# Kernel optimization log

Hardware: AMD Instinct MI355X
Metric: run time of the kernel (lower is better)

## Reference

```python
import jax, jax.numpy as jnp
import numpy as np
from jax import lax

EPS_BN = 1e-5
EPS_LN = 1e-5
IMG = 240
BETA = 1.0

def l2norm(x, axis=-1):
    n = jnp.linalg.norm(x, axis=axis, keepdims=True)
    return x / jnp.maximum(n, 1e-12)

def bn2d(x, g, b):
    # training-mode BatchNorm2d: stats over (B,H,W), biased variance
    m = x.mean(axis=(0, 2, 3), keepdims=True)
    v = x.var(axis=(0, 2, 3), keepdims=True)
    return g[None, :, None, None] * (x - m) * lax.rsqrt(v + EPS_BN) + b[None, :, None, None]

def conv2d(x, w):
    return lax.conv_general_dilated(x, w, (1, 1), 'SAME', dimension_numbers=('NCHW', 'OIHW', 'NCHW'))

def convT2x2(x, w, b):
    # ConvTranspose2d k=2 s=2 pad=0; torch weight layout (C_in, C_out, 2, 2)
    B, C, H, W = x.shape
    O = w.shape[1]
    y = jnp.einsum('bchw,copq->bohpwq', x, w).reshape(B, O, 2 * H, 2 * W)
    return y + b[None, :, None, None]

def layernorm(x, g, b):
    m = x.mean(-1, keepdims=True)
    v = x.var(-1, keepdims=True)
    return g * (x - m) * lax.rsqrt(v + EPS_LN) + b

def setup_inputs() -> dict:
    key = jax.random.key(0)
    ks = jax.random.split(key, 12)
    L, B, K, N, D = 3, 16, 8, 256, 768
    H, MID = 128, 64
    inp = {
        'query': jax.random.normal(ks[0], (L, B, N, D), jnp.float32),
        'prompt': jax.random.normal(ks[1], (L, B, K, N, D), jnp.float32),
        'sharebn_g': jnp.ones((L, D)), 'sharebn_b': jnp.zeros((L, D)),
        'lw1': 0.02 * jax.random.normal(ks[2], (L, H, D, 3, 3)),
        'lbn1g': jnp.ones((L, H)), 'lbn1b': jnp.zeros((L, H)),
        'lwt1': 0.05 * jax.random.normal(ks[3], (L, H, H, 2, 2)), 'lbt1': jnp.zeros((L, H)),
        'lw2': 0.02 * jax.random.normal(ks[4], (L, MID, H, 3, 3)),
        'lbn2g': jnp.ones((L, MID)), 'lbn2b': jnp.zeros((L, MID)),
        'lwt2': 0.05 * jax.random.normal(ks[5], (L, MID, MID, 2, 2)), 'lbt2': jnp.zeros((L, MID)),
        'lw3': 0.05 * jax.random.normal(ks[6], (L, 2, MID, 1, 1)), 'lb3': jnp.zeros((L, 2)),
        'pool_logits': jnp.zeros((L, 2)),
        'mw1': 0.02 * jax.random.normal(ks[7], (L, H, D)),
        'mlng': jnp.ones((L, H)), 'mlnb': jnp.zeros((L, H)),
        'mw2': 0.05 * jax.random.normal(ks[8], (L, 2, H)), 'mb2': jnp.zeros((L, 2)),
    }
    return inp

def _layer(q, pf, p):
    # q: [B,N,D], pf: [B,M,D]
    B, N, D = q.shape
    g = int(N ** 0.5)
    qn = l2norm(q)
    pn = l2norm(pf)
    sim = jnp.einsum('bnc,bmc->bnm', qn, pn)              # [B,N,M]
    max_cos = sim.max(axis=-1)
    idx = sim.argmax(axis=-1)                              # [B,N]
    aligned = jnp.take_along_axis(pf, idx[:, :, None], axis=1)  # [B,N,D]
    residual = 0.5 * (1.0 - max_cos)
    an = l2norm(aligned)
    ctx = qn + BETA * jnp.abs(qn - an)                     # [B,N,D]
    cmap = ctx.transpose(0, 2, 1).reshape(B, D, g, g)
    cmap = bn2d(cmap, p['sbg'], p['sbb'])
    # local conv head
    x = jax.nn.relu(bn2d(conv2d(cmap, p['w1']), p['bn1g'], p['bn1b']))
    x = convT2x2(x, p['wt1'], p['bt1'])
    x = jax.nn.relu(bn2d(conv2d(x, p['w2']), p['bn2g'], p['bn2b']))
    x = convT2x2(x, p['wt2'], p['bt2'])
    raw = conv2d(x, p['w3']) + p['b3'][None, :, None, None]   # [B,2,4g,4g]
    # adaptive_avg_pool2d 4g -> g (exact 4x4 blocks)
    pl2c = raw.reshape(B, 2, g, 4, g, 4).mean(axis=(3, 5))    # [B,2,g,g]
    ps2c = jax.nn.softmax(pl2c, axis=1)
    patch_logits = (pl2c[:, 1] - pl2c[:, 0]).reshape(B, -1)
    patch_scores = ps2c[:, 1].reshape(B, -1)
    local_logits = jax.image.resize(raw, (B, 2, IMG, IMG), method='bilinear')
    # global head (GAP/GMP fusion over context map features)
    cf = cmap.reshape(B, D, N)
    gap = cf.mean(axis=-1)
    gmp = cf.max(axis=-1)
    pw = jax.nn.softmax(p['pl'])
    pooled = pw[0] * gap + pw[1] * gmp                     # [B,D]
    h = jax.nn.relu(layernorm(pooled @ p['mw1'].T, p['lng'], p['lnb']))
    logits2 = h @ p['mw2'].T + p['mb2']
    glogit = logits2[:, 1] - logits2[:, 0]
    return residual, patch_scores, patch_logits, glogit, local_logits, pw, idx, aligned

def reference(query, prompt, sharebn_g, sharebn_b, lw1, lbn1g, lbn1b, lwt1, lbt1,
              lw2, lbn2g, lbn2b, lwt2, lbt2, lw3, lb3, pool_logits,
              mw1, mlng, mlnb, mw2, mb2):
    L, B = query.shape[0], query.shape[1]
    outs = []
    for l in range(L):
        pf = prompt[l].reshape(B, -1, prompt.shape[-1])
        p = dict(sbg=sharebn_g[l], sbb=sharebn_b[l], w1=lw1[l], bn1g=lbn1g[l], bn1b=lbn1b[l],
                 wt1=lwt1[l], bt1=lbt1[l], w2=lw2[l], bn2g=lbn2g[l], bn2b=lbn2b[l],
                 wt2=lwt2[l], bt2=lbt2[l], w3=lw3[l], b3=lb3[l], pl=pool_logits[l],
                 mw1=mw1[l], lng=mlng[l], lnb=mlnb[l], mw2=mw2[l], mb2=mb2[l])
        outs.append(_layer(query[l], pf, p))
    stacked = tuple(jnp.stack([o[i] for o in outs]) for i in range(8))
    return stacked
```

## Files before the change

### kernel.cpp

```cpp
#include <hip/hip_runtime.h>
#include <hip/hip_bf16.h>
#include <math.h>

#define LLY 3
#define BB 16
#define NNQ 256
#define DD 768
#define MMP 2048
#define HH 128
#define MD 64
#define IMGSZ 240
#define LBTOT (LLY*BB)

#define OFF_INVQ 0
#define OFF_INVP (OFF_INVQ + LLY*BB*NNQ)
#define OFF_CMAP (OFF_INVP + LLY*BB*MMP)
#define OFF_BNSH (OFF_CMAP + LLY*BB*DD*NNQ)
#define OFF_X1   (OFF_BNSH + 2*LLY*DD)
#define OFF_BN1  (OFF_X1 + LLY*BB*HH*256)
#define OFF_T1   (OFF_BN1 + 2*LLY*HH)
#define OFF_X2   (OFF_T1 + LLY*BB*HH*1024)
#define OFF_BN2  (OFF_X2 + LLY*BB*MD*1024)
#define OFF_T2   (OFF_BN2 + 2*LLY*MD)
#define OFF_RAW3 (OFF_T2 + LLY*BB*MD*4096)
#define WS_FLOATS (OFF_RAW3 + LLY*BB*2*4096)
#define T1BSH (LBTOT*1024*HH)
#define SQH   (LBTOT*NNQ*DD)
#define OFF_C1P (OFF_T2 + 4718592)
#define OFF_C2P (OFF_T2 + 3256320)
#define OFF_PGL 0
#define X1B_SH 0
#define WT1B_SH 1600000

#define O_RES 0
#define O_PSC (O_RES + LLY*BB*NNQ)
#define O_PLG (O_PSC + LLY*BB*NNQ)
#define O_GLG (O_PLG + LLY*BB*NNQ)
#define O_LOC (O_GLG + LLY*BB)
#define O_PW  (O_LOC + LLY*BB*2*IMGSZ*IMGSZ)
#define O_IDX (O_PW + LLY*2)
#define O_ALN (O_IDX + LLY*BB*NNQ)

typedef __attribute__((ext_vector_type(8))) short bf16x8;
typedef __attribute__((ext_vector_type(4))) float f32x4;

__device__ __forceinline__ unsigned short f2bf(float f) {
    __hip_bfloat16 h = __float2bfloat16(f);
    unsigned short u;
    __builtin_memcpy(&u, &h, sizeof(u));
    return u;
}
__device__ __forceinline__ float bf2f(unsigned short h) {
    return __uint_as_float(((unsigned int)h) << 16);
}

__device__ __forceinline__ float blockReduceSum(float v, float* sm) {
    for (int o = 32; o; o >>= 1) v += __shfl_down(v, o, 64);
    __syncthreads();
    if ((threadIdx.x & 63) == 0) sm[threadIdx.x >> 6] = v;
    __syncthreads();
    return sm[0] + sm[1] + sm[2] + sm[3];
}

__global__ __launch_bounds__(192) void knormq(const float* __restrict__ query,
                                              float* __restrict__ ws) {
    __shared__ float sm[3];
    int row = blockIdx.x;
    int t = threadIdx.x;
    float4 v = *(const float4*)(query + (size_t)row * DD + t * 4);
    float ss = v.x * v.x + v.y * v.y + v.z * v.z + v.w * v.w;
    for (int o = 32; o; o >>= 1) ss += __shfl_down(ss, o, 64);
    if ((t & 63) == 0) sm[t >> 6] = ss;
    __syncthreads();
    ss = sm[0] + sm[1] + sm[2];
    float iv = 1.0f / fmaxf(sqrtf(ss), 1e-12f);
    if (t == 0) ws[OFF_INVQ + row] = iv;
    unsigned short* qh = (unsigned short*)(ws + OFF_T2);
    unsigned short* ql = qh + SQH;
    float e[4] = {v.x * iv, v.y * iv, v.z * iv, v.w * iv};
    unsigned int hp[2], lp[2];
    #pragma unroll
    for (int j = 0; j < 2; j++) {
        unsigned short h0 = f2bf(e[2*j]), h1 = f2bf(e[2*j+1]);
        unsigned short l0 = f2bf(e[2*j] - bf2f(h0)), l1 = f2bf(e[2*j+1] - bf2f(h1));
        hp[j] = (unsigned int)h0 | ((unsigned int)h1 << 16);
        lp[j] = (unsigned int)l0 | ((unsigned int)l1 << 16);
    }
    *(uint2*)(qh + (size_t)row * DD + t * 4) = make_uint2(hp[0], hp[1]);
    *(uint2*)(ql + (size_t)row * DD + t * 4) = make_uint2(lp[0], lp[1]);
}

__global__ __launch_bounds__(512) void ksimm(const float* __restrict__ prompt, float* __restrict__ ws) {
    __shared__ __align__(16) unsigned short Ah[128][40];
    __shared__ __align__(16) unsigned short Al[128][40];
    __shared__ __align__(16) unsigned short Bh[256][40];
    __shared__ __align__(16) unsigned short Bl[256][40];
    __shared__ float invL[128];
    int bid = blockIdx.x;
    int mt = bid & 15;
    int lb = bid >> 4;
    int t = threadIdx.x;
    int lane = t & 63, wave = t >> 6;
    int wm = wave >> 2, wn = wave & 3;
    int fr = lane & 15, fq = lane >> 4;
    const unsigned short* qh = (const unsigned short*)(ws + OFF_T2);
    const unsigned short* ql = qh + SQH;
    const float* pbase = prompt + (size_t)lb * MMP * DD + (size_t)(mt * 128) * DD;

    float ssq[2] = {0.f, 0.f};

    f32x4 acc[4][4];
    #pragma unroll
    for (int mi = 0; mi < 4; mi++)
        #pragma unroll
        for (int ni = 0; ni < 4; ni++) acc[mi][ni] = (f32x4){0.f, 0.f, 0.f, 0.f};

    for (int kc = 0; kc < DD; kc += 32) {
        __syncthreads();
        #pragma unroll
        for (int i = 0; i < 2; i++) {
            int f = t + i * 512;
            int row = f >> 3, c4 = f & 7;
            float4 v = *(const float4*)(pbase + (size_t)row * DD + kc + c4 * 4);
            ssq[i] += v.x * v.x + v.y * v.y + v.z * v.z + v.w * v.w;
            unsigned short h0 = f2bf(v.x), h1 = f2bf(v.y), h2 = f2bf(v.z), h3 = f2bf(v.w);
            unsigned short l0 = f2bf(v.x - bf2f(h0)), l1 = f2bf(v.y - bf2f(h1));
            unsigned short l2 = f2bf(v.z - bf2f(h2)), l3 = f2bf(v.w - bf2f(h3));
            uint2 hp = make_uint2((unsigned int)h0 | ((unsigned int)h1 << 16),
                                  (unsigned int)h2 | ((unsigned int)h3 << 16));
            uint2 lp = make_uint2((unsigned int)l0 | ((unsigned int)l1 << 16),
                                  (unsigned int)l2 | ((unsigned int)l3 << 16));
            *(uint2*)&Ah[row][c4 * 4] = hp;
            *(uint2*)&Al[row][c4 * 4] = lp;
        }
        #pragma unroll
        for (int i = 0; i < 2; i++) {
            int f = t + i * 512;
            int row = f >> 2, sg = f & 3;
            size_t go = (size_t)(lb * NNQ + row) * DD + kc + sg * 8;
            *(uint4*)&Bh[row][sg * 8] = *(const uint4*)(qh + go);
            *(uint4*)&Bl[row][sg * 8] = *(const uint4*)(ql + go);
        }
        __syncthreads();
        bf16x8 ah[4], al4[4], bh[4], bl4[4];
        #pragma unroll
        for (int mi = 0; mi < 4; mi++) {
            ah[mi]  = *(const bf16x8*)&Ah[wm * 64 + mi * 16 + fr][fq * 8];
            al4[mi] = *(const bf16x8*)&Al[wm * 64 + mi * 16 + fr][fq * 8];
        }
        #pragma unroll
        for (int ni = 0; ni < 4; ni++) {
            bh[ni]  = *(const bf16x8*)&Bh[wn * 64 + ni * 16 + fr][fq * 8];
            bl4[ni] = *(const bf16x8*)&Bl[wn * 64 + ni * 16 + fr][fq * 8];
        }
        #pragma unroll
        for (int mi = 0; mi < 4; mi++)
            #pragma unroll
            for (int ni = 0; ni < 4; ni++) {
                acc[mi][ni] = __builtin_amdgcn_mfma_f32_16x16x32_bf16(ah[mi],  bh[ni],  acc[mi][ni], 0, 0, 0);
                acc[mi][ni] = __builtin_amdgcn_mfma_f32_16x16x32_bf16(ah[mi],  bl4[ni], acc[mi][ni], 0, 0, 0);
                acc[mi][ni] = __builtin_amdgcn_mfma_f32_16x16x32_bf16(al4[mi], bh[ni],  acc[mi][ni], 0, 0, 0);
            }
    }
    #pragma unroll
    for (int i = 0; i < 2; i++) {
        float s = ssq[i];
        s += __shfl_xor(s, 1, 64);
        s += __shfl_xor(s, 2, 64);
        s += __shfl_xor(s, 4, 64);
        if ((t & 7) == 0) {
            int row = (t >> 3) + 64 * i;
            float iv = 1.0f / fmaxf(sqrtf(s), 1e-12f);
            invL[row] = iv;
            ws[OFF_INVP + lb * MMP + mt * 128 + row] = iv;
        }
    }
    __syncthreads();
    float* bestv = ws + OFF_X1;
    float* besti = ws + OFF_X1 + (size_t)LBTOT * NNQ * 32;
    #pragma unroll
    for (int ni = 0; ni < 4; ni++) {
        float bv = -1e30f; int bi = 0;
        #pragma unroll
        for (int mi = 0; mi < 4; mi++)
            #pragma unroll
            for (int rr = 0; rr < 4; rr++) {
                int lm = wm * 64 + mi * 16 + fq * 4 + rr;
                float s = acc[mi][ni][rr] * invL[lm];
                int m = mt * 128 + lm;
                if (s > bv) { bv = s; bi = m; }
            }
        #pragma unroll
        for (int o = 16; o <= 32; o <<= 1) {
            float ov = __shfl_xor(bv, o, 64);
            int oi = __shfl_xor(bi, o, 64);
            if (ov > bv || (ov == bv && oi < bi)) { bv = ov; bi = oi; }
        }
        if (fq == 0) {
            int q = wn * 64 + ni * 16 + fr;
            size_t slot = (size_t)(lb * NNQ + q) * 32 + wm * 16 + mt;
            bestv[slot] = bv;
            besti[slot] = (float)bi;
        }
    }
}

__global__ __launch_bounds__(256) void kpost(const float* __restrict__ query,
                                             const float* __restrict__ prompt,
                                             float* __restrict__ ws,
                                             float* __restrict__ out) {
    __shared__ float red_v[16];
    __shared__ int   red_i[16];
    __shared__ float Lctx[DD * 17];
    int bid = blockIdx.x;
    int nt = bid & 15;
    int lb = bid >> 4;
    int t = threadIdx.x;
    const float* bestv = ws + OFF_X1;
    const float* besti = ws + OFF_X1 + (size_t)LBTOT * NNQ * 32;
    if (t < 16) {
        int q = nt * 16 + t;
        const float* bv = bestv + (size_t)(lb * NNQ + q) * 32;
        const float* bi = besti + (size_t)(lb * NNQ + q) * 32;
        float best = -1e30f; int bidx2 = 0;
        for (int mtt = 0; mtt < 16; mtt++)
            #pragma unroll
            for (int wm = 0; wm < 2; wm++) {
                float v = bv[wm * 16 + mtt];
                if (v > best) { best = v; bidx2 = (int)bi[wm * 16 + mtt]; }
            }
        red_v[t] = best; red_i[t] = bidx2;
        out[O_RES + lb * NNQ + q] = 0.5f * (1.0f - best);
        out[O_IDX + lb * NNQ + q] = (float)bidx2;
    }
    __syncthreads();
    const float* qbase = query + (size_t)(lb * NNQ + nt * 16) * DD;
    const float* pbase = prompt + (size_t)lb * MMP * DD;
    const float* invq = ws + OFF_INVQ + lb * NNQ + nt * 16;
    const float* invp = ws + OFF_INVP + lb * MMP;
    int c = t & 15;
    int nn = t >> 4;
    int gn = nt * 16 + nn;
    int midx = red_i[nn];
    float ip = invp[midx];
    float iq = invq[nn];
    const float* prow = pbase + (size_t)midx * DD;
    const float* qrow = qbase + (size_t)nn * DD;
    float* aln = out + O_ALN + (size_t)(lb * NNQ + gn) * DD;
    for (int jj = 0; jj < DD / 16; jj++) {
        int d = c + jj * 16;
        float pvr = prow[d];
        float qv = qrow[d] * iq;
        float av = pvr * ip;
        float cx = qv + fabsf(qv - av);
        aln[d] = pvr;
        Lctx[d * 17 + nn] = cx;
    }
    __syncthreads();
    float* cm = ws + OFF_CMAP + (size_t)lb * DD * NNQ + nt * 16;
    int nl = t & 15, dd = t >> 4;
    for (int jj = 0; jj < DD / 16; jj++) {
        int d = jj * 16 + dd;
        cm[(size_t)d * NNQ + nl] = Lctx[d * 17 + nl];
    }
    {
        float* pp = ws + OFF_C1P + (size_t)(lb * 16 + nt) * (DD * 4);
        #pragma unroll
        for (int k = 0; k < 3; k++) {
            int d = t * 3 + k;
            float s = 0.f, sq = 0.f, mx = -1e30f, mn = 1e30f;
            #pragma unroll
            for (int n2 = 0; n2 < 16; n2++) {
                float v = Lctx[d * 17 + n2];
                s += v; sq += v * v;
                mx = fmaxf(mx, v); mn = fminf(mn, v);
            }
            pp[d] = s;
            pp[DD + d] = sq;
            pp[2 * DD + d] = mx;
            pp[3 * DD + d] = mn;
        }
    }
}

__global__ __launch_bounds__(256) void kbnfin(const float* __restrict__ g,
                                              const float* __restrict__ b,
                                              float* __restrict__ ws) {
    __shared__ float ssm[4][64], sqm[4][64];
    int chunk = blockIdx.x % 12;
    int l = blockIdx.x / 12;
    int t = threadIdx.x;
    int d = chunk * 64 + (t & 63);
    int r = t >> 6;
    float s = 0.f, sq = 0.f;
    for (int j = r; j < 256; j += 4) {
        const float* pp = ws + OFF_C1P + (size_t)(l * 256 + j) * (DD * 4);
        s += pp[d];
        sq += pp[DD + d];
    }
    ssm[r][t & 63] = s; sqm[r][t & 63] = sq;
    __syncthreads();
    if (r == 0) {
        s  = ssm[0][t] + ssm[1][t] + ssm[2][t] + ssm[3][t];
        sq = sqm[0][t] + sqm[1][t] + sqm[2][t] + sqm[3][t];
        float inv = 1.0f / 4096.f;
        float m = s * inv;
        float var = sq * inv - m * m;
        float sc = g[l * DD + d] * rsqrtf(var + 1e-5f);
        float bo = b[l * DD + d] - m * sc;
        ws[OFF_BNSH + l * DD + d] = sc;
        ws[OFF_BNSH + LLY * DD + l * DD + d] = bo;
    }
}

__global__ __launch_bounds__(64) void kgapf(float* __restrict__ ws,
                                            const float* __restrict__ pool_logits) {
    int chunk = blockIdx.x % 12;
    int lb = blockIdx.x / 12;
    int l = lb >> 4;
    int t = threadIdx.x;
    int d = chunk * 64 + t;
    float s = 0.f, mx = -1e30f, mn = 1e30f;
    for (int nt = 0; nt < 16; nt++) {
        const float* pp = ws + OFF_C1P + (size_t)(lb * 16 + nt) * (DD * 4);
        s += pp[d];
        mx = fmaxf(mx, pp[2 * DD + d]);
        mn = fminf(mn, pp[3 * DD + d]);
    }
    float p0 = pool_logits[l * 2], p1 = pool_logits[l * 2 + 1];
    float mxp = fmaxf(p0, p1);
    float e0 = expf(p0 - mxp), e1 = expf(p1 - mxp);
    float pw0 = e0 / (e0 + e1), pw1 = e1 / (e0 + e1);
    float sc = ws[OFF_BNSH + l * DD + d];
    float bo = ws[OFF_BNSH + LLY * DD + l * DD + d];
    float gap = sc * (s * (1.f / NNQ)) + bo;
    float gmp = (sc >= 0.f) ? (sc * mx + bo) : (sc * mn + bo);
    ws[OFF_PGL + lb * DD + d] = pw0 * gap + pw1 * gmp;
}

__global__ __launch_bounds__(256) void kbnstats(const float* __restrict__ x, int C, int SP,
                                                const float* __restrict__ g,
                                                const float* __restrict__ b,
                                                float* __restrict__ outSB) {
    __shared__ float sm[4];
    int bid = blockIdx.x;
    int c = bid % C;
    int l = bid / C;
    int t = threadIdx.x;
    float s = 0.f, sq = 0.f;
    for (int bb2 = 0; bb2 < BB; ++bb2) {
        const float* p = x + ((size_t)(l * BB + bb2) * C + c) * SP;
        for (int i = t; i < SP; i += 256) { float v = p[i]; s += v; sq += v * v; }
    }
    s = blockReduceSum(s, sm);
    sq = blockReduceSum(sq, sm);
    if (t == 0) {
        float inv = 1.0f / (float)(BB * SP);
        float m = s * inv;
        float var = sq * inv - m * m;
        float sc = g[l * C + c] * rsqrtf(var + 1e-5f);
        float bo = b[l * C + c] - m * sc;
        outSB[l * C + c] = sc;
        outSB[LLY * C + l * C + c] = bo;
    }
}

__global__ __launch_bounds__(256) void kw1cvt(const float* __restrict__ lw1, float* __restrict__ ws) {
    unsigned short* w1B = (unsigned short*)(ws + OFF_X2);
    int bid = blockIdx.x;
    int l = bid / HH, co = bid % HH;
    int t = threadIdx.x;
    for (int c0 = 0; c0 < DD; c0 += 256) {
        int ci = c0 + t;
        const float* src = lw1 + ((size_t)(l * HH + co) * DD + ci) * 9;
        #pragma unroll
        for (int tap = 0; tap < 9; tap++) {
            w1B[((size_t)((l * 9 + tap) * HH + co)) * DD + ci] = f2bf(src[tap]);
        }
    }
}

__global__ __launch_bounds__(256) void kbn1cvt(float* __restrict__ ws) {
    __shared__ float Ld[64][65];
    unsigned short* cmT = (unsigned short*)(ws + OFF_T2);
    int bid = blockIdx.x;
    int nt = bid & 3;
    int r = bid >> 2;
    int ct = r % 12;
    int lb = r / 12;
    int l = lb >> 4;
    int t = threadIdx.x;
    const float* cmap = ws + OFF_CMAP + (size_t)lb * DD * NNQ;
    const float* bns = ws + OFF_BNSH + l * DD;
    const float* bnb = ws + OFF_BNSH + LLY * DD + l * DD;
    #pragma unroll
    for (int i = 0; i < 4; i++) {
        int f = t + i * 256;
        int row = f >> 4, c4 = f & 15;
        int ci = ct * 64 + row;
        float4 v = *(const float4*)(cmap + (size_t)ci * NNQ + nt * 64 + c4 * 4);
        float s = bns[ci], bo = bnb[ci];
        Ld[row][c4*4+0] = v.x * s + bo; Ld[row][c4*4+1] = v.y * s + bo;
        Ld[row][c4*4+2] = v.z * s + bo; Ld[row][c4*4+3] = v.w * s + bo;
    }
    __syncthreads();
    #pragma unroll
    for (int i = 0; i < 2; i++) {
        int f = t + i * 256;
        int row = f >> 3, seg = f & 7;
        unsigned int pk[4];
        #pragma unroll
        for (int e = 0; e < 4; e++) {
            unsigned int lo = f2bf(Ld[seg * 8 + 2 * e][row]);
            unsigned int hi = f2bf(Ld[seg * 8 + 2 * e + 1][row]);
            pk[e] = lo | (hi << 16);
        }
        uint4 o = make_uint4(pk[0], pk[1], pk[2], pk[3]);
        *(uint4*)(cmT + ((size_t)(lb * NNQ + nt * 64 + row)) * DD + ct * 64 + seg * 8) = o;
    }
}

__global__ __launch_bounds__(256) void kconv1m(float* __restrict__ ws) {
    __shared__ __align__(16) unsigned short Ab[128][72];
    __shared__ __align__(16) unsigned short Bb[128][72];
    int bid = blockIdx.x;
    int s = bid % 6;
    int ntile = (bid / 6) & 1;
    int lb = bid / 12;
    int l = lb >> 4;
    int t = threadIdx.x;
    int lane = t & 63;
    int wave = t >> 6;
    int wr = wave >> 1, wc = wave & 1;
    int fr = lane & 15, fq = lane >> 4;
    const unsigned short* w1B = (const unsigned short*)(ws + OFF_X2);
    const unsigned short* cmT = (const unsigned short*)(ws + OFF_T2);

    f32x4 acc[4][4];
    #pragma unroll
    for (int mi = 0; mi < 4; mi++)
        #pragma unroll
        for (int ni = 0; ni < 4; ni++) acc[mi][ni] = (f32x4){0.f, 0.f, 0.f, 0.f};

    for (int g = s * 18; g < s * 18 + 18; ++g) {
        int tap = g / 12;
        int kc = (g % 12) * 64;
        int dy = tap / 3 - 1, dx = tap % 3 - 1;
        const unsigned short* wpl = w1B + (size_t)((l * 9 + tap) * HH) * DD;
        __syncthreads();
        #pragma unroll
        for (int i = 0; i < 4; i++) {
            int f = t + i * 256;
            int row = f >> 3, seg = f & 7;
            uint4 v = *(const uint4*)(wpl + (size_t)row * DD + kc + seg * 8);
            *(uint4*)&Ab[row][seg * 8] = v;
        }
        #pragma unroll
        for (int i = 0; i < 4; i++) {
            int f = t + i * 256;
            int row = f >> 3, seg = f & 7;
            int n = ntile * 128 + row;
            int y = (n >> 4) + dy, x = (n & 15) + dx;
            bool ok = ((unsigned)y < 16u) && ((unsigned)x < 16u);
            uint4 v = make_uint4(0u, 0u, 0u, 0u);
            if (ok) v = *(const uint4*)(cmT + ((size_t)(lb * NNQ + y * 16 + x)) * DD + kc + seg * 8);
            *(uint4*)&Bb[row][seg * 8] = v;
        }
        __syncthreads();
        #pragma unroll
        for (int kk = 0; kk < 64; kk += 32) {
            bf16x8 af[4], bfv[4];
            #pragma unroll
            for (int mi = 0; mi < 4; mi++)
                af[mi] = *(const bf16x8*)&Ab[wr * 64 + mi * 16 + fr][kk + fq * 8];
            #pragma unroll
            for (int ni = 0; ni < 4; ni++)
                bfv[ni] = *(const bf16x8*)&Bb[wc * 64 + ni * 16 + fr][kk + fq * 8];
            #pragma unroll
            for (int mi = 0; mi < 4; mi++)
                #pragma unroll
                for (int ni = 0; ni < 4; ni++)
                    acc[mi][ni] = __builtin_amdgcn_mfma_f32_16x16x32_bf16(af[mi], bfv[ni], acc[mi][ni], 0, 0, 0);
        }
    }
    float* dst = (s == 5) ? (ws + OFF_X1 + (size_t)lb * HH * 256)
                          : (ws + OFF_C1P + (size_t)(s * LBTOT + lb) * (HH * 256));
    #pragma unroll
    for (int mi = 0; mi < 4; mi++) {
        #pragma unroll
        for (int ni = 0; ni < 4; ni++) {
            int gn = ntile * 128 + wc * 64 + ni * 16 + fr;
            #pragma unroll
            for (int rr = 0; rr < 4; rr++) {
                int co = wr * 64 + mi * 16 + fq * 4 + rr;
                dst[(size_t)co * 256 + gn] = acc[mi][ni][rr];
            }
        }
    }
}

__global__ __launch_bounds__(256) void kc1red(float* __restrict__ ws) {
    size_t i = ((size_t)blockIdx.x * 256 + threadIdx.x) * 8;
    float4 a0 = *(float4*)(ws + OFF_X1 + i);
    float4 a1 = *(float4*)(ws + OFF_X1 + i + 4);
    #pragma unroll
    for (int s = 0; s < 5; s++) {
        const float* p = ws + OFF_C1P + (size_t)s * (LBTOT * HH * 256) + i;
        float4 b0 = *(const float4*)p;
        float4 b1 = *(const float4*)(p + 4);
        a0.x += b0.x; a0.y += b0.y; a0.z += b0.z; a0.w += b0.w;
        a1.x += b1.x; a1.y += b1.y; a1.z += b1.z; a1.w += b1.w;
    }
    *(float4*)(ws + OFF_X1 + i) = a0;
    *(float4*)(ws + OFF_X1 + i + 4) = a1;
}

__global__ __launch_bounds__(256) void kxcvt(const float* __restrict__ x,
                                             const float* __restrict__ sbsb,
                                             unsigned short* __restrict__ xb,
                                             int CI, int SPIN, int nT, int cT) {
    __shared__ float Ld[64][65];
    int bid = blockIdx.x;
    int nt = bid % nT;
    int r = bid / nT;
    int ct = r % cT;
    int lb = r / cT;
    int l = lb >> 4;
    int t = threadIdx.x;
    const float* sc = sbsb + l * CI;
    const float* bo = sbsb + LLY * CI + l * CI;
    #pragma unroll
    for (int i = 0; i < 4; i++) {
        int f = t + i * 256;
        int row = f >> 4, c4 = f & 15;
        int ci = ct * 64 + row;
        float4 v = *(const float4*)(x + ((size_t)lb * CI + ci) * SPIN + nt * 64 + c4 * 4);
        float s = sc[ci], b_ = bo[ci];
        Ld[row][c4*4+0] = fmaxf(v.x * s + b_, 0.f);
        Ld[row][c4*4+1] = fmaxf(v.y * s + b_, 0.f);
        Ld[row][c4*4+2] = fmaxf(v.z * s + b_, 0.f);
        Ld[row][c4*4+3] = fmaxf(v.w * s + b_, 0.f);
    }
    __syncthreads();
    int segs = CI >> 3;
    for (int f = t; f < 64 * segs; f += 256) {
        int row = f / segs, seg = f % segs;
        int sl = seg - ct * 8;
        if (sl < 0 || sl >= 8) continue;
        unsigned int pk[4];
        #pragma unroll
        for (int e = 0; e < 4; e++) {
            unsigned int lo = f2bf(Ld[sl * 8 + 2 * e][row]);
            unsigned int hi = f2bf(Ld[sl * 8 + 2 * e + 1][row]);
            pk[e] = lo | (hi << 16);
        }
        uint4 o = make_uint4(pk[0], pk[1], pk[2], pk[3]);
        *(uint4*)(xb + ((size_t)lb * SPIN + nt * 64 + row) * CI + ct * 64 + sl * 8) = o;
    }
}

__global__ __launch_bounds__(128) void kwtcvt(const float* __restrict__ lwt,
                                              unsigned short* __restrict__ dst,
                                              int CI, int CO) {
    int bid = blockIdx.x;
    int l = bid / CO, co = bid % CO;
    int t = threadIdx.x;
    if (t < CI) {
        const float* src = lwt + (((size_t)(l * CI + t) * CO + co) * 4);
        #pragma unroll
        for (int pq = 0; pq < 4; pq++) {
            dst[((size_t)((l * 4 + pq) * CO + co)) * CI + t] = f2bf(src[pq]);
        }
    }
}

__global__ __launch_bounds__(256) void kconvTm(const unsigned short* __restrict__ xb,
                                               const unsigned short* __restrict__ wtb,
                                               const float* __restrict__ bt,
                                               float* __restrict__ xout,
                                               int CI, int CO, int gsh, int nTiles, int coTiles) {
    __shared__ __align__(16) unsigned short Ab[64][72];
    __shared__ __align__(16) unsigned short Bb[256][72];
    int bid = blockIdx.x;
    int ntile = bid % nTiles;
    int r = bid / nTiles;
    int cot = r % coTiles; r /= coTiles;
    int pq = r & 3;
    int lb = r >> 2;
    int l = lb >> 4;
    int SPIN = 1 << (2 * gsh);
    int t = threadIdx.x, lane = t & 63, wave = t >> 6;
    int fr = lane & 15, fq = lane >> 4;

    f32x4 acc[4][4];
    #pragma unroll
    for (int mi = 0; mi < 4; mi++)
        #pragma unroll
        for (int ni = 0; ni < 4; ni++) acc[mi][ni] = (f32x4){0.f, 0.f, 0.f, 0.f};

    for (int kc = 0; kc < CI; kc += 64) {
        __syncthreads();
        #pragma unroll
        for (int i = 0; i < 2; i++) {
            int f = t + i * 256;
            int row = f >> 3, seg = f & 7;
            *(uint4*)&Ab[row][seg * 8] =
                *(const uint4*)(wtb + ((size_t)((l * 4 + pq) * CO + cot * 64 + row)) * CI + kc + seg * 8);
        }
        #pragma unroll
        for (int i = 0; i < 8; i++) {
            int f = t + i * 256;
            int row = f >> 3, seg = f & 7;
            *(uint4*)&Bb[row][seg * 8] =
                *(const uint4*)(xb + ((size_t)lb * SPIN + ntile * 256 + row) * CI + kc + seg * 8);
        }
        __syncthreads();
        #pragma unroll
        for (int kk = 0; kk < 64; kk += 32) {
            bf16x8 af[4], bfv[4];
            #pragma unroll
            for (int mi = 0; mi < 4; mi++)
                af[mi] = *(const bf16x8*)&Ab[mi * 16 + fr][kk + fq * 8];
            #pragma unroll
            for (int ni = 0; ni < 4; ni++)
                bfv[ni] = *(const bf16x8*)&Bb[wave * 64 + ni * 16 + fr][kk + fq * 8];
            #pragma unroll
            for (int mi = 0; mi < 4; mi++)
                #pragma unroll
                for (int ni = 0; ni < 4; ni++)
                    acc[mi][ni] = __builtin_amdgcn_mfma_f32_16x16x32_bf16(af[mi], bfv[ni], acc[mi][ni], 0, 0, 0);
        }
    }
    int p = pq >> 1, q = pq & 1;
    int GIN = 1 << gsh;
    #pragma unroll
    for (int mi = 0; mi < 4; mi++) {
        #pragma unroll
        for (int rr = 0; rr < 4; rr++) {
            int co = cot * 64 + mi * 16 + fq * 4 + rr;
            float bias = bt[l * CO + co];
            float* orow = xout + ((size_t)(lb * CO + co)) * (4 * SPIN);
            #pragma unroll
            for (int ni = 0; ni < 4; ni++) {
                int n = ntile * 256 + wave * 64 + ni * 16 + fr;
                int h = n >> gsh, w = n & (GIN - 1);
                orow[(2 * h + p) * (2 * GIN) + 2 * w + q] = acc[mi][ni][rr] + bias;
            }
        }
    }
}

__global__ __launch_bounds__(256) void kconvT2f(const unsigned short* __restrict__ xb,
                                                const unsigned short* __restrict__ wtb,
                                                const float* __restrict__ bt,
                                                const float* __restrict__ lw3,
                                                const float* __restrict__ lb3,
                                                float* __restrict__ ws) {
    __shared__ __align__(16) unsigned short Ab[64][72];
    __shared__ __align__(16) unsigned short Bb[256][72];
    __shared__ float w3s[2][64];
    int bid = blockIdx.x;
    int ntile = bid & 3;
    int r = bid >> 2;
    int pq = r & 3;
    int lb = r >> 2;
    int l = lb >> 4;
    const int CI = MD, CO = MD, gsh = 5;
    int SPIN = 1 << (2 * gsh);
    int t = threadIdx.x, lane = t & 63, wave = t >> 6;
    int fr = lane & 15, fq = lane >> 4;
    if (t < 128) w3s[t >> 6][t & 63] = lw3[(size_t)(l * 2 + (t >> 6)) * MD + (t & 63)];

    f32x4 acc[4][4];
    #pragma unroll
    for (int mi = 0; mi < 4; mi++)
        #pragma unroll
        for (int ni = 0; ni < 4; ni++) acc[mi][ni] = (f32x4){0.f, 0.f, 0.f, 0.f};

    __syncthreads();
    #pragma unroll
    for (int i = 0; i < 2; i++) {
        int f = t + i * 256;
        int row = f >> 3, seg = f & 7;
        *(uint4*)&Ab[row][seg * 8] =
            *(const uint4*)(wtb + ((size_t)((l * 4 + pq) * CO + row)) * CI + seg * 8);
    }
    #pragma unroll
    for (int i = 0; i < 8; i++) {
        int f = t + i * 256;
        int row = f >> 3, seg = f & 7;
        *(uint4*)&Bb[row][seg * 8] =
            *(const uint4*)(xb + ((size_t)lb * SPIN + ntile * 256 + row) * CI + seg * 8);
    }
    __syncthreads();
    #pragma unroll
    for (int kk = 0; kk < 64; kk += 32) {
        bf16x8 af[4], bfv[4];
        #pragma unroll
        for (int mi = 0; mi < 4; mi++)
            af[mi] = *(const bf16x8*)&Ab[mi * 16 + fr][kk + fq * 8];
        #pragma unroll
        for (int ni = 0; ni < 4; ni++)
            bfv[ni] = *(const bf16x8*)&Bb[wave * 64 + ni * 16 + fr][kk + fq * 8];
        #pragma unroll
        for (int mi = 0; mi < 4; mi++)
            #pragma unroll
            for (int ni = 0; ni < 4; ni++)
                acc[mi][ni] = __builtin_amdgcn_mfma_f32_16x16x32_bf16(af[mi], bfv[ni], acc[mi][ni], 0, 0, 0);
    }
    float s0[4] = {0.f, 0.f, 0.f, 0.f};
    float s1[4] = {0.f, 0.f, 0.f, 0.f};
    #pragma unroll
    for (int mi = 0; mi < 4; mi++) {
        #pragma unroll
        for (int rr = 0; rr < 4; rr++) {
            int co = mi * 16 + fq * 4 + rr;
            float bias = bt[l * CO + co];
            float w0 = w3s[0][co], w1 = w3s[1][co];
            #pragma unroll
            for (int ni = 0; ni < 4; ni++) {
                float val = acc[mi][ni][rr] + bias;
                s0[ni] += w0 * val;
                s1[ni] += w1 * val;
            }
        }
    }
    #pragma unroll
    for (int ni = 0; ni < 4; ni++) {
        s0[ni] += __shfl_xor(s0[ni], 16, 64); s0[ni] += __shfl_xor(s0[ni], 32, 64);
        s1[ni] += __shfl_xor(s1[ni], 16, 64); s1[ni] += __shfl_xor(s1[ni], 32, 64);
    }
    if (fq == 0) {
        int p = pq >> 1, q = pq & 1;
        float* r3 = ws + OFF_RAW3 + (size_t)lb * 2 * 4096;
        float b30 = lb3[l * 2], b31 = lb3[l * 2 + 1];
        #pragma unroll
        for (int ni = 0; ni < 4; ni++) {
            int n = ntile * 256 + wave * 64 + ni * 16 + fr;
            int h = n >> 5, w = n & 31;
            int opix = (2 * h + p) * 64 + 2 * w + q;
            r3[opix] = s0[ni] + b30;
            r3[4096 + opix] = s1[ni] + b31;
        }
    }
}

__global__ __launch_bounds__(256) void kt1cvt(float* __restrict__ ws) {
    __shared__ float Ld[64][65];
    unsigned short* t1B = (unsigned short*)(ws + OFF_T2);
    int bid = blockIdx.x;
    int ntile = bid & 15;
    int r = bid >> 4;
    int ct = r & 1;
    int lb = r >> 1;
    int t = threadIdx.x;
    const float* t1p = ws + OFF_T1 + (size_t)lb * HH * 1024;
    #pragma unroll
    for (int i = 0; i < 4; i++) {
        int f = t + i * 256;
        int row = f >> 4, c4 = f & 15;
        float4 v = *(const float4*)(t1p + (size_t)(ct * 64 + row) * 1024 + ntile * 64 + c4 * 4);
        *(float4*)&Ld[row][c4 * 4] = v;
    }
    __syncthreads();
    #pragma unroll
    for (int i = 0; i < 2; i++) {
        int f = t + i * 256;
        int row = f >> 3, seg = f & 7;
        unsigned int pk[4];
        #pragma unroll
        for (int e = 0; e < 4; e++) {
            unsigned int lo = f2bf(Ld[seg * 8 + 2 * e][row]);
            unsigned int hi = f2bf(Ld[seg * 8 + 2 * e + 1][row]);
            pk[e] = lo | (hi << 16);
        }
        uint4 o = make_uint4(pk[0], pk[1], pk[2], pk[3]);
        *(uint4*)(t1B + ((size_t)(lb * 1024 + ntile * 64 + row)) * HH + ct * 64 + seg * 8) = o;
    }
}

__global__ __launch_bounds__(256) void kw2cvt(const float* __restrict__ lw2, float* __restrict__ ws) {
    unsigned short* w2B = (unsigned short*)(ws + OFF_T2) + T1BSH;
    int bid = blockIdx.x;
    int l = bid / MD, co = bid % MD;
    int t = threadIdx.x;
    if (t < HH) {
        int ci = t;
        const float* src = lw2 + ((size_t)(l * MD + co) * HH + ci) * 9;
        #pragma unroll
        for (int tap = 0; tap < 9; tap++) {
            w2B[((size_t)((l * 9 + tap) * MD + co)) * HH + ci] = f2bf(src[tap]);
        }
    }
}

__global__ __launch_bounds__(256) void kconv2m(float* __restrict__ ws) {
    __shared__ __align__(16) unsigned short Ab[64][72];
    __shared__ __align__(16) unsigned short Bb[256][72];
    int bid = blockIdx.x;
    int s = bid & 1;
    int ntile = (bid >> 1) & 3;
    int lb = bid >> 3;
    int l = lb >> 4;
    int t = threadIdx.x;
    int lane = t & 63;
    int wave = t >> 6;
    int fr = lane & 15, fq = lane >> 4;
    const unsigned short* t1B = (const unsigned short*)(ws + OFF_T2);
    const unsigned short* w2B = (const unsigned short*)(ws + OFF_T2) + T1BSH;

    f32x4 acc[4][4];
    #pragma unroll
    for (int mi = 0; mi < 4; mi++)
        #pragma unroll
        for (int ni = 0; ni < 4; ni++) acc[mi][ni] = (f32x4){0.f, 0.f, 0.f, 0.f};

    for (int g = s * 9; g < s * 9 + 9; ++g) {
        int tap = g >> 1;
        int kc = (g & 1) * 64;
        int dy = tap / 3 - 1, dx = tap % 3 - 1;
        const unsigned short* wpl = w2B + (size_t)((l * 9 + tap) * MD) * HH;
        __syncthreads();
        #pragma unroll
        for (int i = 0; i < 2; i++) {
            int f = t + i * 256;
            int row = f >> 3, seg = f & 7;
            uint4 v = *(const uint4*)(wpl + (size_t)row * HH + kc + seg * 8);
            *(uint4*)&Ab[row][seg * 8] = v;
        }
        #pragma unroll
        for (int i = 0; i < 8; i++) {
            int f = t + i * 256;
            int row = f >> 3, seg = f & 7;
            int n = ntile * 256 + row;
            int y = (n >> 5) + dy, x = (n & 31) + dx;
            bool ok = ((unsigned)y < 32u) && ((unsigned)x < 32u);
            uint4 v = make_uint4(0u, 0u, 0u, 0u);
            if (ok) v = *(const uint4*)(t1B + ((size_t)(lb * 1024 + y * 32 + x)) * HH + kc + seg * 8);
            *(uint4*)&Bb[row][seg * 8] = v;
        }
        __syncthreads();
        #pragma unroll
        for (int kk = 0; kk < 64; kk += 32) {
            bf16x8 af[4], bfv[4];
            #pragma unroll
            for (int mi = 0; mi < 4; mi++)
                af[mi] = *(const bf16x8*)&Ab[mi * 16 + fr][kk + fq * 8];
            #pragma unroll
            for (int ni = 0; ni < 4; ni++)
                bfv[ni] = *(const bf16x8*)&Bb[wave * 64 + ni * 16 + fr][kk + fq * 8];
            #pragma unroll
            for (int mi = 0; mi < 4; mi++)
                #pragma unroll
                for (int ni = 0; ni < 4; ni++)
                    acc[mi][ni] = __builtin_amdgcn_mfma_f32_16x16x32_bf16(af[mi], bfv[ni], acc[mi][ni], 0, 0, 0);
        }
    }
    float* dst = (s == 1) ? (ws + OFF_X2 + (size_t)lb * MD * 1024)
                          : (ws + OFF_C2P + (size_t)lb * MD * 1024);
    #pragma unroll
    for (int mi = 0; mi < 4; mi++) {
        #pragma unroll
        for (int ni = 0; ni < 4; ni++) {
            int gn = ntile * 256 + wave * 64 + ni * 16 + fr;
            #pragma unroll
            for (int rr = 0; rr < 4; rr++) {
                int co = mi * 16 + fq * 4 + rr;
                dst[(size_t)co * 1024 + gn] = acc[mi][ni][rr];
            }
        }
    }
}

__global__ __launch_bounds__(256) void kc2red(float* __restrict__ ws) {
    size_t i = ((size_t)blockIdx.x * 256 + threadIdx.x) * 8;
    float4 a0 = *(float4*)(ws + OFF_X2 + i);
    float4 a1 = *(float4*)(ws + OFF_X2 + i + 4);
    const float* p = ws + OFF_C2P + i;
    float4 b0 = *(const float4*)p;
    float4 b1 = *(const float4*)(p + 4);
    a0.x += b0.x; a0.y += b0.y; a0.z += b0.z; a0.w += b0.w;
    a1.x += b1.x; a1.y += b1.y; a1.z += b1.z; a1.w += b1.w;
    *(float4*)(ws + OFF_X2 + i) = a0;
    *(float4*)(ws + OFF_X2 + i + 4) = a1;
}

__global__ __launch_bounds__(256) void kpool(const float* __restrict__ ws, float* __restrict__ out) {
    int lb = blockIdx.x;
    int t = threadIdx.x;
    int gy = t >> 4, gx = t & 15;
    const float* r3 = ws + OFF_RAW3 + (size_t)lb * 2 * 4096;
    float pl[2];
    #pragma unroll
    for (int ch = 0; ch < 2; ch++) {
        const float* basep = r3 + ch * 4096;
        float s = 0.f;
        #pragma unroll
        for (int dy = 0; dy < 4; dy++)
            #pragma unroll
            for (int dx = 0; dx < 4; dx++)
                s += basep[(gy * 4 + dy) * 64 + gx * 4 + dx];
        pl[ch] = s * (1.f / 16.f);
    }
    out[O_PLG + lb * NNQ + t] = pl[1] - pl[0];
    out[O_PSC + lb * NNQ + t] = 1.f / (1.f + expf(pl[0] - pl[1]));
}

__global__ __launch_bounds__(256) void kresize(const float* __restrict__ ws, float* __restrict__ out) {
    int id = blockIdx.x * 256 + threadIdx.x;
    int ox = id % IMGSZ;
    int tmp = id / IMGSZ;
    int oy = tmp % IMGSZ;
    int tmp2 = tmp / IMGSZ;
    int ch = tmp2 & 1;
    int lb = tmp2 >> 1;
    const float S = 64.f / 240.f;
    float xs = fminf(fmaxf((ox + 0.5f) * S - 0.5f, 0.f), 63.f);
    float ys = fminf(fmaxf((oy + 0.5f) * S - 0.5f, 0.f), 63.f);
    int x0 = (int)xs, y0 = (int)ys;
    float fx = xs - x0, fy = ys - y0;
    int x1 = min(x0 + 1, 63), y1 = min(y0 + 1, 63);
    const float* basep = ws + OFF_RAW3 + (size_t)(lb * 2 + ch) * 4096;
    float v00 = basep[y0 * 64 + x0], v01 = basep[y0 * 64 + x1];
    float v10 = basep[y1 * 64 + x0], v11 = basep[y1 * 64 + x1];
    float v = (1.f - fy) * ((1.f - fx) * v00 + fx * v01) + fy * ((1.f - fx) * v10 + fx * v11);
    out[O_LOC + id] = v;
}

__global__ __launch_bounds__(256) void kglob2(const float* __restrict__ ws,
                                              const float* __restrict__ pool_logits,
                                              const float* __restrict__ mw1,
                                              const float* __restrict__ mlng,
                                              const float* __restrict__ mlnb,
                                              const float* __restrict__ mw2,
                                              const float* __restrict__ mb2,
                                              float* __restrict__ out) {
    __shared__ float pooled[DD];
    __shared__ float zbuf[HH];
    __shared__ float hbuf[HH];
    __shared__ float sm[4];
    int lb = blockIdx.x;
    int l = lb >> 4;
    int b = lb & 15;
    int t = threadIdx.x;
    float p0 = pool_logits[l * 2], p1 = pool_logits[l * 2 + 1];
    float mx = fmaxf(p0, p1);
    float e0 = expf(p0 - mx), e1 = expf(p1 - mx);
    float pw0 = e0 / (e0 + e1), pw1 = e1 / (e0 + e1);
    if (b == 0 && t < 2) out[O_PW + l * 2 + t] = (t == 0) ? pw0 : pw1;

    for (int d = t; d < DD; d += 256) pooled[d] = ws[OFF_PGL + lb * DD + d];
    __syncthreads();
    if (t < HH) {
        const float* wrow = mw1 + (size_t)(l * HH + t) * DD;
        float a = 0.f;
        for (int d2 = 0; d2 < DD; d2++) a += pooled[d2] * wrow[d2];
        zbuf[t] = a;
    }
    __syncthreads();
    float zv = (t < HH) ? zbuf[t] : 0.f;
    float s1r = blockReduceSum(zv, sm);
    float s2r = blockReduceSum(zv * zv, sm);
    float mean = s1r * (1.f / HH);
    float var = s2r * (1.f / HH) - mean * mean;
    float rstd = rsqrtf(var + 1e-5f);
    if (t < HH) {
        float h = (zbuf[t] - mean) * rstd * mlng[l * HH + t] + mlnb[l * HH + t];
        hbuf[t] = fmaxf(h, 0.f);
    }
    __syncthreads();
    float hv = (t < HH) ? hbuf[t] : 0.f;
    float w0v = (t < HH) ? mw2[(size_t)(l * 2 + 0) * HH + t] : 0.f;
    float w1v = (t < HH) ? mw2[(size_t)(l * 2 + 1) * HH + t] : 0.f;
    float s0 = blockReduceSum(hv * w0v, sm);
    float s1 = blockReduceSum(hv * w1v, sm);
    if (t == 0) out[O_GLG + lb] = (s1 + mb2[l * 2 + 1]) - (s0 + mb2[l * 2]);
}

extern "C" void kernel_launch(void* const* d_in, const int* in_sizes, int n_in,
                              void* d_out, int out_size, void* d_ws, size_t ws_size,
                              hipStream_t stream) {
    const float* query      = (const float*)d_in[0];
    const float* prompt     = (const float*)d_in[1];
    const float* sharebn_g  = (const float*)d_in[2];
    const float* sharebn_b  = (const float*)d_in[3];
    const float* lw1        = (const float*)d_in[4];
    const float* lbn1g      = (const float*)d_in[5];
    const float* lbn1b      = (const float*)d_in[6];
    const float* lwt1       = (const float*)d_in[7];
    const float* lbt1       = (const float*)d_in[8];
    const float* lw2        = (const float*)d_in[9];
    const float* lbn2g      = (const float*)d_in[10];
    const float* lbn2b      = (const float*)d_in[11];
    const float* lwt2       = (const float*)d_in[12];
    const float* lbt2       = (const float*)d_in[13];
    const float* lw3        = (const float*)d_in[14];
    const float* lb3        = (const float*)d_in[15];
    const float* pool_logits= (const float*)d_in[16];
    const float* mw1        = (const float*)d_in[17];
    const float* mlng       = (const float*)d_in[18];
    const float* mlnb       = (const float*)d_in[19];
    const float* mw2        = (const float*)d_in[20];
    const float* mb2        = (const float*)d_in[21];
    float* out = (float*)d_out;
    float* ws = (float*)d_ws;

    hipLaunchKernelGGL(knormq, dim3(LLY*BB*NNQ), dim3(192), 0, stream, query, ws);
    hipLaunchKernelGGL(ksimm, dim3(LBTOT*16), dim3(512), 0, stream, prompt, ws);
    hipLaunchKernelGGL(kpost, dim3(LBTOT*16), dim3(256), 0, stream, query, prompt, ws, out);
    hipLaunchKernelGGL(kbnfin, dim3(LLY*12), dim3(256), 0, stream, sharebn_g, sharebn_b, ws);
    hipLaunchKernelGGL(kgapf, dim3(LBTOT*12), dim3(64), 0, stream, ws, pool_logits);
    hipLaunchKernelGGL(kw1cvt, dim3(LLY*HH), dim3(256), 0, stream, lw1, ws);
    hipLaunchKernelGGL(kbn1cvt, dim3(LBTOT*48), dim3(256), 0, stream, ws);
    hipLaunchKernelGGL(kconv1m, dim3(LBTOT*12), dim3(256), 0, stream, ws);
    hipLaunchKernelGGL(kc1red, dim3(768), dim3(256), 0, stream, ws);
    hipLaunchKernelGGL(kbnstats, dim3(LLY*HH), dim3(256), 0, stream,
                       ws + OFF_X1, HH, 256, lbn1g, lbn1b, ws + OFF_BN1);
    hipLaunchKernelGGL(kxcvt, dim3(LBTOT*8), dim3(256), 0, stream,
                       ws + OFF_X1, ws + OFF_BN1, (unsigned short*)(ws + OFF_T2) + X1B_SH,
                       HH, 256, 4, 2);
    hipLaunchKernelGGL(kwtcvt, dim3(LLY*HH), dim3(128), 0, stream,
                       lwt1, (unsigned short*)(ws + OFF_T2) + WT1B_SH, HH, HH);
    hipLaunchKernelGGL(kconvTm, dim3(LBTOT*4*2), dim3(256), 0, stream,
                       (const unsigned short*)(ws + OFF_T2) + X1B_SH,
                       (const unsigned short*)(ws + OFF_T2) + WT1B_SH,
                       lbt1, ws + OFF_T1, HH, HH, 4, 1, 2);
    hipLaunchKernelGGL(kt1cvt, dim3(LBTOT*32), dim3(256), 0, stream, ws);
    hipLaunchKernelGGL(kw2cvt, dim3(LLY*MD), dim3(256), 0, stream, lw2, ws);
    hipLaunchKernelGGL(kconv2m, dim3(LBTOT*8), dim3(256), 0, stream, ws);
    hipLaunchKernelGGL(kc2red, dim3(1536), dim3(256), 0, stream, ws);
    hipLaunchKernelGGL(kbnstats, dim3(LLY*MD), dim3(256), 0, stream,
                       ws + OFF_X2, MD, 1024, lbn2g, lbn2b, ws + OFF_BN2);
    hipLaunchKernelGGL(kxcvt, dim3(LBTOT*16), dim3(256), 0, stream,
                       ws + OFF_X2, ws + OFF_BN2, (unsigned short*)(ws + OFF_X1),
                       MD, 1024, 16, 1);
    hipLaunchKernelGGL(kwtcvt, dim3(LLY*MD), dim3(128), 0, stream,
                       lwt2, (unsigned short*)(ws + OFF_X2), MD, MD);
    hipLaunchKernelGGL(kconvT2f, dim3(LBTOT*4*4), dim3(256), 0, stream,
                       (const unsigned short*)(ws + OFF_X1),
                       (const unsigned short*)(ws + OFF_X2),
                       lbt2, lw3, lb3, ws);
    hipLaunchKernelGGL(kpool, dim3(LBTOT), dim3(256), 0, stream, ws, out);
    hipLaunchKernelGGL(kresize, dim3(LLY*BB*2*IMGSZ*IMGSZ/256), dim3(256), 0, stream, ws, out);
    hipLaunchKernelGGL(kglob2, dim3(LBTOT), dim3(256), 0, stream,
                       ws, pool_logits, mw1, mlng, mlnb, mw2, mb2, out);
}
```

Before: 494.0 us.

## Fuse small pipeline kernels and fold split-K reductions into consumers

Merges several small launches: BN finalize with GAP/GMP pooling, activation/weight conversions into combined grids, and the resize/pool/global-head tail into one kernel. The separate split-K reduction kernels for conv1 and conv2 are removed. Their partial sums are instead added inside the BN-stats and conversion kernels, which both re-read the partials. This cuts launch count and one write/read pass over the conv outputs, at the cost of duplicated partial-sum reads and a relocated ConvT2 weight buffer in the workspace.

```diff
diff --git a/kernel.cpp b/kernel.cpp
--- a/kernel.cpp
+++ b/kernel.cpp
@@ -29,6 +29,7 @@
 #define OFF_C1P (OFF_T2 + 4718592)
 #define OFF_C2P (OFF_T2 + 3256320)
 #define OFF_PGL 0
+#define OFF_WT2B 60000
 #define X1B_SH 0
 #define WT1B_SH 1600000
 
@@ -40,6 +41,8 @@
 #define O_PW  (O_LOC + LLY*BB*2*IMGSZ*IMGSZ)
 #define O_IDX (O_PW + LLY*2)
 #define O_ALN (O_IDX + LLY*BB*NNQ)
+
+#define NRESB (LLY*BB*2*IMGSZ*IMGSZ/256)
 
 typedef __attribute__((ext_vector_type(8))) short bf16x8;
 typedef __attribute__((ext_vector_type(4))) float f32x4;
@@ -283,12 +286,14 @@
     }
 }
 
-__global__ __launch_bounds__(256) void kbnfin(const float* __restrict__ g,
-                                              const float* __restrict__ b,
-                                              float* __restrict__ ws) {
-    __shared__ float ssm[4][64], sqm[4][64];
+__global__ __launch_bounds__(256) void kstatsgap(const float* __restrict__ g,
+                                                 const float* __restrict__ b,
+                                                 const float* __restrict__ pool_logits,
+                                                 float* __restrict__ ws) {
+    __shared__ float ssm[4][64], sqm[4][64], scs[64], bos[64];
     int chunk = blockIdx.x % 12;
-    int l = blockIdx.x / 12;
+    int lb = blockIdx.x / 12;
+    int l = lb >> 4;
     int t = threadIdx.x;
     int d = chunk * 64 + (t & 63);
     int r = t >> 6;
@@ -310,35 +315,32 @@
         float bo = b[l * DD + d] - m * sc;
         ws[OFF_BNSH + l * DD + d] = sc;
         ws[OFF_BNSH + LLY * DD + l * DD + d] = bo;
-    }
-}
-
-__global__ __launch_bounds__(64) void kgapf(float* __restrict__ ws,
-                                            const float* __restrict__ pool_logits) {
-    int chunk = blockIdx.x % 12;
-    int lb = blockIdx.x / 12;
-    int l = lb >> 4;
-    int t = threadIdx.x;
-    int d = chunk * 64 + t;
-    float s = 0.f, mx = -1e30f, mn = 1e30f;
-    for (int nt = 0; nt < 16; nt++) {
-        const float* pp = ws + OFF_C1P + (size_t)(lb * 16 + nt) * (DD * 4);
-        s += pp[d];
-        mx = fmaxf(mx, pp[2 * DD + d]);
-        mn = fminf(mn, pp[3 * DD + d]);
-    }
-    float p0 = pool_logits[l * 2], p1 = pool_logits[l * 2 + 1];
-    float mxp = fmaxf(p0, p1);
-    float e0 = expf(p0 - mxp), e1 = expf(p1 - mxp);
-    float pw0 = e0 / (e0 + e1), pw1 = e1 / (e0 + e1);
-    float sc = ws[OFF_BNSH + l * DD + d];
-    float bo = ws[OFF_BNSH + LLY * DD + l * DD + d];
-    float gap = sc * (s * (1.f / NNQ)) + bo;
-    float gmp = (sc >= 0.f) ? (sc * mx + bo) : (sc * mn + bo);
-    ws[OFF_PGL + lb * DD + d] = pw0 * gap + pw1 * gmp;
-}
-
-__global__ __launch_bounds__(256) void kbnstats(const float* __restrict__ x, int C, int SP,
+        scs[t] = sc; bos[t] = bo;
+    }
+    __syncthreads();
+    if (r == 0) {
+        float s2 = 0.f, mx = -1e30f, mn = 1e30f;
+        for (int nt = 0; nt < 16; nt++) {
+            const float* pp = ws + OFF_C1P + (size_t)(lb * 16 + nt) * (DD * 4);
+            s2 += pp[d];
+            mx = fmaxf(mx, pp[2 * DD + d]);
+            mn = fminf(mn, pp[3 * DD + d]);
+        }
+        float p0 = pool_logits[l * 2], p1 = pool_logits[l * 2 + 1];
+        float mxp = fmaxf(p0, p1);
+        float e0 = expf(p0 - mxp), e1 = expf(p1 - mxp);
+        float pw0 = e0 / (e0 + e1), pw1 = e1 / (e0 + e1);
+        float sc = scs[t], bo = bos[t];
+        float gap = sc * (s2 * (1.f / NNQ)) + bo;
+        float gmp = (sc >= 0.f) ? (sc * mx + bo) : (sc * mn + bo);
+        ws[OFF_PGL + lb * DD + d] = pw0 * gap + pw1 * gmp;
+    }
+}
+
+__global__ __launch_bounds__(256) void kbnstats(const float* __restrict__ x,
+                                                const float* __restrict__ parts,
+                                                int npart, size_t pstride,
+                                                int C, int SP,
                                                 const float* __restrict__ g,
                                                 const float* __restrict__ b,
                                                 float* __restrict__ outSB) {
@@ -349,8 +351,12 @@
     int t = threadIdx.x;
     float s = 0.f, sq = 0.f;
     for (int bb2 = 0; bb2 < BB; ++bb2) {
-        const float* p = x + ((size_t)(l * BB + bb2) * C + c) * SP;
-        for (int i = t; i < SP; i += 256) { float v = p[i]; s += v; sq += v * v; }
+        size_t base = ((size_t)(l * BB + bb2) * C + c) * SP;
+        for (int i = t; i < SP; i += 256) {
+            float v = x[base + i];
+            for (int s2 = 0; s2 < npart; s2++) v += parts[pstride * s2 + base + i];
+            s += v; sq += v * v;
+        }
     }
     s = blockReduceSum(s, sm);
     sq = blockReduceSum(sq, sm);
@@ -499,34 +505,18 @@
     }
 }
 
-__global__ __launch_bounds__(256) void kc1red(float* __restrict__ ws) {
-    size_t i = ((size_t)blockIdx.x * 256 + threadIdx.x) * 8;
-    float4 a0 = *(float4*)(ws + OFF_X1 + i);
-    float4 a1 = *(float4*)(ws + OFF_X1 + i + 4);
-    #pragma unroll
-    for (int s = 0; s < 5; s++) {
-        const float* p = ws + OFF_C1P + (size_t)s * (LBTOT * HH * 256) + i;
-        float4 b0 = *(const float4*)p;
-        float4 b1 = *(const float4*)(p + 4);
-        a0.x += b0.x; a0.y += b0.y; a0.z += b0.z; a0.w += b0.w;
-        a1.x += b1.x; a1.y += b1.y; a1.z += b1.z; a1.w += b1.w;
-    }
-    *(float4*)(ws + OFF_X1 + i) = a0;
-    *(float4*)(ws + OFF_X1 + i + 4) = a1;
-}
-
-__global__ __launch_bounds__(256) void kxcvt(const float* __restrict__ x,
-                                             const float* __restrict__ sbsb,
-                                             unsigned short* __restrict__ xb,
-                                             int CI, int SPIN, int nT, int cT) {
-    __shared__ float Ld[64][65];
-    int bid = blockIdx.x;
+__device__ __forceinline__ void xcvt_body(const float* __restrict__ x,
+                                          const float* __restrict__ parts,
+                                          int npart, size_t pstride,
+                                          const float* __restrict__ sbsb,
+                                          unsigned short* __restrict__ xb,
+                                          int CI, int SPIN, int nT, int cT,
+                                          int bid, int t, float Ld[64][65]) {
     int nt = bid % nT;
     int r = bid / nT;
     int ct = r % cT;
     int lb = r / cT;
     int l = lb >> 4;
-    int t = threadIdx.x;
     const float* sc = sbsb + l * CI;
     const float* bo = sbsb + LLY * CI + l * CI;
     #pragma unroll
@@ -534,12 +524,17 @@
         int f = t + i * 256;
         int row = f >> 4, c4 = f & 15;
         int ci = ct * 64 + row;
-        float4 v = *(const float4*)(x + ((size_t)lb * CI + ci) * SPIN + nt * 64 + c4 * 4);
-        float s = sc[ci], b_ = bo[ci];
-        Ld[row][c4*4+0] = fmaxf(v.x * s + b_, 0.f);
-        Ld[row][c4*4+1] = fmaxf(v.y * s + b_, 0.f);
-        Ld[row][c4*4+2] = fmaxf(v.z * s + b_, 0.f);
-        Ld[row][c4*4+3] = fmaxf(v.w * s + b_, 0.f);
+        size_t idx = ((size_t)lb * CI + ci) * SPIN + nt * 64 + c4 * 4;
+        float4 v = *(const float4*)(x + idx);
+        for (int s = 0; s < npart; s++) {
+            float4 pv = *(const float4*)(parts + pstride * s + idx);
+            v.x += pv.x; v.y += pv.y; v.z += pv.z; v.w += pv.w;
+        }
+        float s_ = sc[ci], b_ = bo[ci];
+        Ld[row][c4*4+0] = fmaxf(v.x * s_ + b_, 0.f);
+        Ld[row][c4*4+1] = fmaxf(v.y * s_ + b_, 0.f);
+        Ld[row][c4*4+2] = fmaxf(v.z * s_ + b_, 0.f);
+        Ld[row][c4*4+3] = fmaxf(v.w * s_ + b_, 0.f);
     }
     __syncthreads();
     int segs = CI >> 3;
@@ -559,18 +554,30 @@
     }
 }
 
-__global__ __launch_bounds__(128) void kwtcvt(const float* __restrict__ lwt,
-                                              unsigned short* __restrict__ dst,
-                                              int CI, int CO) {
-    int bid = blockIdx.x;
+__device__ __forceinline__ void wtcvt_body(const float* __restrict__ lwt,
+                                           unsigned short* __restrict__ dst,
+                                           int CI, int CO, int bid, int t) {
     int l = bid / CO, co = bid % CO;
-    int t = threadIdx.x;
     if (t < CI) {
         const float* src = lwt + (((size_t)(l * CI + t) * CO + co) * 4);
         #pragma unroll
         for (int pq = 0; pq < 4; pq++) {
             dst[((size_t)((l * 4 + pq) * CO + co)) * CI + t] = f2bf(src[pq]);
         }
+    }
+}
+
+__global__ __launch_bounds__(256) void kcvtT1(const float* __restrict__ lwt1,
+                                              float* __restrict__ ws) {
+    __shared__ float Ld[64][65];
+    int bid = blockIdx.x, t = threadIdx.x;
+    if (bid < LBTOT * 8) {
+        xcvt_body(ws + OFF_X1, ws + OFF_C1P, 5, (size_t)LBTOT * HH * 256,
+                  ws + OFF_BN1, (unsigned short*)(ws + OFF_T2) + X1B_SH,
+                  HH, 256, 4, 2, bid, t, Ld);
+    } else {
+        wtcvt_body(lwt1, (unsigned short*)(ws + OFF_T2) + WT1B_SH, HH, HH,
+                   bid - LBTOT * 8, t);
     }
 }
 
@@ -647,6 +654,146 @@
                 orow[(2 * h + p) * (2 * GIN) + 2 * w + q] = acc[mi][ni][rr] + bias;
             }
         }
+    }
+}
+
+__global__ __launch_bounds__(256) void kcvtT2mix(const float* __restrict__ lw2,
+                                                 float* __restrict__ ws) {
+    __shared__ float Ld[64][65];
+    int bid = blockIdx.x, t = threadIdx.x;
+    if (bid < LBTOT * 32) {
+        unsigned short* t1B = (unsigned short*)(ws + OFF_T2);
+        int ntile = bid & 15;
+        int r = bid >> 4;
+        int ct = r & 1;
+        int lb = r >> 1;
+        const float* t1p = ws + OFF_T1 + (size_t)lb * HH * 1024;
+        #pragma unroll
+        for (int i = 0; i < 4; i++) {
+            int f = t + i * 256;
+            int row = f >> 4, c4 = f & 15;
+            float4 v = *(const float4*)(t1p + (size_t)(ct * 64 + row) * 1024 + ntile * 64 + c4 * 4);
+            *(float4*)&Ld[row][c4 * 4] = v;
+        }
+        __syncthreads();
+        #pragma unroll
+        for (int i = 0; i < 2; i++) {
+            int f = t + i * 256;
+            int row = f >> 3, seg = f & 7;
+            unsigned int pk[4];
+            #pragma unroll
+            for (int e = 0; e < 4; e++) {
+                unsigned int lo = f2bf(Ld[seg * 8 + 2 * e][row]);
+                unsigned int hi = f2bf(Ld[seg * 8 + 2 * e + 1][row]);
+                pk[e] = lo | (hi << 16);
+            }
+            uint4 o = make_uint4(pk[0], pk[1], pk[2], pk[3]);
+            *(uint4*)(t1B + ((size_t)(lb * 1024 + ntile * 64 + row)) * HH + ct * 64 + seg * 8) = o;
+        }
+    } else {
+        unsigned short* w2B = (unsigned short*)(ws + OFF_T2) + T1BSH;
+        int wb = bid - LBTOT * 32;
+        int l = wb / MD, co = wb % MD;
+        if (t < HH) {
+            int ci = t;
+            const float* src = lw2 + ((size_t)(l * MD + co) * HH + ci) * 9;
+            #pragma unroll
+            for (int tap = 0; tap < 9; tap++) {
+                w2B[((size_t)((l * 9 + tap) * MD + co)) * HH + ci] = f2bf(src[tap]);
+            }
+        }
+    }
+}
+
+__global__ __launch_bounds__(256) void kconv2m(float* __restrict__ ws) {
+    __shared__ __align__(16) unsigned short Ab[64][72];
+    __shared__ __align__(16) unsigned short Bb[256][72];
+    int bid = blockIdx.x;
+    int s = bid & 1;
+    int ntile = (bid >> 1) & 3;
+    int lb = bid >> 3;
+    int l = lb >> 4;
+    int t = threadIdx.x;
+    int lane = t & 63;
+    int wave = t >> 6;
+    int fr = lane & 15, fq = lane >> 4;
+    const unsigned short* t1B = (const unsigned short*)(ws + OFF_T2);
+    const unsigned short* w2B = (const unsigned short*)(ws + OFF_T2) + T1BSH;
+
+    f32x4 acc[4][4];
+    #pragma unroll
+    for (int mi = 0; mi < 4; mi++)
+        #pragma unroll
+        for (int ni = 0; ni < 4; ni++) acc[mi][ni] = (f32x4){0.f, 0.f, 0.f, 0.f};
+
+    for (int g = s * 9; g < s * 9 + 9; ++g) {
+        int tap = g >> 1;
+        int kc = (g & 1) * 64;
+        int dy = tap / 3 - 1, dx = tap % 3 - 1;
+        const unsigned short* wpl = w2B + (size_t)((l * 9 + tap) * MD) * HH;
+        __syncthreads();
+        #pragma unroll
+        for (int i = 0; i < 2; i++) {
+            int f = t + i * 256;
+            int row = f >> 3, seg = f & 7;
+            uint4 v = *(const uint4*)(wpl + (size_t)row * HH + kc + seg * 8);
+            *(uint4*)&Ab[row][seg * 8] = v;
+        }
+        #pragma unroll
+        for (int i = 0; i < 8; i++) {
+            int f = t + i * 256;
+            int row = f >> 3, seg = f & 7;
+            int n = ntile * 256 + row;
+            int y = (n >> 5) + dy, x = (n & 31) + dx;
+            bool ok = ((unsigned)y < 32u) && ((unsigned)x < 32u);
+            uint4 v = make_uint4(0u, 0u, 0u, 0u);
+            if (ok) v = *(const uint4*)(t1B + ((size_t)(lb * 1024 + y * 32 + x)) * HH + kc + seg * 8);
+            *(uint4*)&Bb[row][seg * 8] = v;
+        }
+        __syncthreads();
+        #pragma unroll
+        for (int kk = 0; kk < 64; kk += 32) {
+            bf16x8 af[4], bfv[4];
+            #pragma unroll
+            for (int mi = 0; mi < 4; mi++)
+                af[mi] = *(const bf16x8*)&Ab[mi * 16 + fr][kk + fq * 8];
+            #pragma unroll
+            for (int ni = 0; ni < 4; ni++)
+                bfv[ni] = *(const bf16x8*)&Bb[wave * 64 + ni * 16 + fr][kk + fq * 8];
+            #pragma unroll
+            for (int mi = 0; mi < 4; mi++)
+                #pragma unroll
+                for (int ni = 0; ni < 4; ni++)
+                    acc[mi][ni] = __builtin_amdgcn_mfma_f32_16x16x32_bf16(af[mi], bfv[ni], acc[mi][ni], 0, 0, 0);
+        }
+    }
+    float* dst = (s == 1) ? (ws + OFF_X2 + (size_t)lb * MD * 1024)
+                          : (ws + OFF_C2P + (size_t)lb * MD * 1024);
+    #pragma unroll
+    for (int mi = 0; mi < 4; mi++) {
+        #pragma unroll
+        for (int ni = 0; ni < 4; ni++) {
+            int gn = ntile * 256 + wave * 64 + ni * 16 + fr;
+            #pragma unroll
+            for (int rr = 0; rr < 4; rr++) {
+                int co = mi * 16 + fq * 4 + rr;
+                dst[(size_t)co * 1024 + gn] = acc[mi][ni][rr];
+            }
+        }
+    }
+}
+
+__global__ __launch_bounds__(256) void kcvtT2b(const float* __restrict__ lwt2,
+                                               float* __restrict__ ws) {
+    __shared__ float Ld[64][65];
+    int bid = blockIdx.x, t = threadIdx.x;
+    if (bid < LBTOT * 16) {
+        xcvt_body(ws + OFF_X2, ws + OFF_C2P, 1, (size_t)0,
+                  ws + OFF_BN2, (unsigned short*)(ws + OFF_X1),
+                  MD, 1024, 16, 1, bid, t, Ld);
+    } else {
+        wtcvt_body(lwt2, (unsigned short*)(ws + OFF_WT2B), MD, MD,
+                   bid - LBTOT * 16, t);
     }
 }
 
@@ -745,236 +892,98 @@
     }
 }
 
-__global__ __launch_bounds__(256) void kt1cvt(float* __restrict__ ws) {
-    __shared__ float Ld[64][65];
-    unsigned short* t1B = (unsigned short*)(ws + OFF_T2);
-    int bid = blockIdx.x;
-    int ntile = bid & 15;
-    int r = bid >> 4;
-    int ct = r & 1;
-    int lb = r >> 1;
-    int t = threadIdx.x;
-    const float* t1p = ws + OFF_T1 + (size_t)lb * HH * 1024;
-    #pragma unroll
-    for (int i = 0; i < 4; i++) {
-        int f = t + i * 256;
-        int row = f >> 4, c4 = f & 15;
-        float4 v = *(const float4*)(t1p + (size_t)(ct * 64 + row) * 1024 + ntile * 64 + c4 * 4);
-        *(float4*)&Ld[row][c4 * 4] = v;
-    }
-    __syncthreads();
-    #pragma unroll
-    for (int i = 0; i < 2; i++) {
-        int f = t + i * 256;
-        int row = f >> 3, seg = f & 7;
-        unsigned int pk[4];
-        #pragma unroll
-        for (int e = 0; e < 4; e++) {
-            unsigned int lo = f2bf(Ld[seg * 8 + 2 * e][row]);
-            unsigned int hi = f2bf(Ld[seg * 8 + 2 * e + 1][row]);
-            pk[e] = lo | (hi << 16);
-        }
-        uint4 o = make_uint4(pk[0], pk[1], pk[2], pk[3]);
-        *(uint4*)(t1B + ((size_t)(lb * 1024 + ntile * 64 + row)) * HH + ct * 64 + seg * 8) = o;
-    }
-}
-
-__global__ __launch_bounds__(256) void kw2cvt(const float* __restrict__ lw2, float* __restrict__ ws) {
-    unsigned short* w2B = (unsigned short*)(ws + OFF_T2) + T1BSH;
-    int bid = blockIdx.x;
-    int l = bid / MD, co = bid % MD;
-    int t = threadIdx.x;
-    if (t < HH) {
-        int ci = t;
-        const float* src = lw2 + ((size_t)(l * MD + co) * HH + ci) * 9;
-        #pragma unroll
-        for (int tap = 0; tap < 9; tap++) {
-            w2B[((size_t)((l * 9 + tap) * MD + co)) * HH + ci] = f2bf(src[tap]);
-        }
-    }
-}
-
-__global__ __launch_bounds__(256) void kconv2m(float* __restrict__ ws) {
-    __shared__ __align__(16) unsigned short Ab[64][72];
-    __shared__ __align__(16) unsigned short Bb[256][72];
-    int bid = blockIdx.x;
-    int s = bid & 1;
-    int ntile = (bid >> 1) & 3;
-    int lb = bid >> 3;
-    int l = lb >> 4;
-    int t = threadIdx.x;
-    int lane = t & 63;
-    int wave = t >> 6;
-    int fr = lane & 15, fq = lane >> 4;
-    const unsigned short* t1B = (const unsigned short*)(ws + OFF_T2);
-    const unsigned short* w2B = (const unsigned short*)(ws + OFF_T2) + T1BSH;
-
-    f32x4 acc[4][4];
-    #pragma unroll
-    for (int mi = 0; mi < 4; mi++)
-        #pragma unroll
-        for (int ni = 0; ni < 4; ni++) acc[mi][ni] = (f32x4){0.f, 0.f, 0.f, 0.f};
-
-    for (int g = s * 9; g < s * 9 + 9; ++g) {
-        int tap = g >> 1;
-        int kc = (g & 1) * 64;
-        int dy = tap / 3 - 1, dx = tap % 3 - 1;
-        const unsigned short* wpl = w2B + (size_t)((l * 9 + tap) * MD) * HH;
-        __syncthreads();
-        #pragma unroll
-        for (int i = 0; i < 2; i++) {
-            int f = t + i * 256;
-            int row = f >> 3, seg = f & 7;
-            uint4 v = *(const uint4*)(wpl + (size_t)row * HH + kc + seg * 8);
-            *(uint4*)&Ab[row][seg * 8] = v;
-        }
-        #pragma unroll
-        for (int i = 0; i < 8; i++) {
-            int f = t + i * 256;
-            int row = f >> 3, seg = f & 7;
-            int n = ntile * 256 + row;
-            int y = (n >> 5) + dy, x = (n & 31) + dx;
-            bool ok = ((unsigned)y < 32u) && ((unsigned)x < 32u);
-            uint4 v = make_uint4(0u, 0u, 0u, 0u);
-            if (ok) v = *(const uint4*)(t1B + ((size_t)(lb * 1024 + y * 32 + x)) * HH + kc + seg * 8);
-            *(uint4*)&Bb[row][seg * 8] = v;
-        }
-        __syncthreads();
-        #pragma unroll
-        for (int kk = 0; kk < 64; kk += 32) {
-            bf16x8 af[4], bfv[4];
-            #pragma unroll
-            for (int mi = 0; mi < 4; mi++)
-                af[mi] = *(const bf16x8*)&Ab[mi * 16 + fr][kk + fq * 8];
-            #pragma unroll
-            for (int ni = 0; ni < 4; ni++)
-                bfv[ni] = *(const bf16x8*)&Bb[wave * 64 + ni * 16 + fr][kk + fq * 8];
-            #pragma unroll
-            for (int mi = 0; mi < 4; mi++)
-                #pragma unroll
-                for (int ni = 0; ni < 4; ni++)
-                    acc[mi][ni] = __builtin_amdgcn_mfma_f32_16x16x32_bf16(af[mi], bfv[ni], acc[mi][ni], 0, 0, 0);
-        }
-    }
-    float* dst = (s == 1) ? (ws + OFF_X2 + (size_t)lb * MD * 1024)
-                          : (ws + OFF_C2P + (size_t)lb * MD * 1024);
-    #pragma unroll
-    for (int mi = 0; mi < 4; mi++) {
-        #pragma unroll
-        for (int ni = 0; ni < 4; ni++) {
-            int gn = ntile * 256 + wave * 64 + ni * 16 + fr;
-            #pragma unroll
-            for (int rr = 0; rr < 4; rr++) {
-                int co = mi * 16 + fq * 4 + rr;
-                dst[(size_t)co * 1024 + gn] = acc[mi][ni][rr];
-            }
-        }
-    }
-}
-
-__global__ __launch_bounds__(256) void kc2red(float* __restrict__ ws) {
-    size_t i = ((size_t)blockIdx.x * 256 + threadIdx.x) * 8;
-    float4 a0 = *(float4*)(ws + OFF_X2 + i);
-    float4 a1 = *(float4*)(ws + OFF_X2 + i + 4);
-    const float* p = ws + OFF_C2P + i;
-    float4 b0 = *(const float4*)p;
-    float4 b1 = *(const float4*)(p + 4);
-    a0.x += b0.x; a0.y += b0.y; a0.z += b0.z; a0.w += b0.w;
-    a1.x += b1.x; a1.y += b1.y; a1.z += b1.z; a1.w += b1.w;
-    *(float4*)(ws + OFF_X2 + i) = a0;
-    *(float4*)(ws + OFF_X2 + i + 4) = a1;
-}
-
-__global__ __launch_bounds__(256) void kpool(const float* __restrict__ ws, float* __restrict__ out) {
-    int lb = blockIdx.x;
-    int t = threadIdx.x;
-    int gy = t >> 4, gx = t & 15;
-    const float* r3 = ws + OFF_RAW3 + (size_t)lb * 2 * 4096;
-    float pl[2];
-    #pragma unroll
-    for (int ch = 0; ch < 2; ch++) {
-        const float* basep = r3 + ch * 4096;
-        float s = 0.f;
-        #pragma unroll
-        for (int dy = 0; dy < 4; dy++)
-            #pragma unroll
-            for (int dx = 0; dx < 4; dx++)
-                s += basep[(gy * 4 + dy) * 64 + gx * 4 + dx];
-        pl[ch] = s * (1.f / 16.f);
-    }
-    out[O_PLG + lb * NNQ + t] = pl[1] - pl[0];
-    out[O_PSC + lb * NNQ + t] = 1.f / (1.f + expf(pl[0] - pl[1]));
-}
-
-__global__ __launch_bounds__(256) void kresize(const float* __restrict__ ws, float* __restrict__ out) {
-    int id = blockIdx.x * 256 + threadIdx.x;
-    int ox = id % IMGSZ;
-    int tmp = id / IMGSZ;
-    int oy = tmp % IMGSZ;
-    int tmp2 = tmp / IMGSZ;
-    int ch = tmp2 & 1;
-    int lb = tmp2 >> 1;
-    const float S = 64.f / 240.f;
-    float xs = fminf(fmaxf((ox + 0.5f) * S - 0.5f, 0.f), 63.f);
-    float ys = fminf(fmaxf((oy + 0.5f) * S - 0.5f, 0.f), 63.f);
-    int x0 = (int)xs, y0 = (int)ys;
-    float fx = xs - x0, fy = ys - y0;
-    int x1 = min(x0 + 1, 63), y1 = min(y0 + 1, 63);
-    const float* basep = ws + OFF_RAW3 + (size_t)(lb * 2 + ch) * 4096;
-    float v00 = basep[y0 * 64 + x0], v01 = basep[y0 * 64 + x1];
-    float v10 = basep[y1 * 64 + x0], v11 = basep[y1 * 64 + x1];
-    float v = (1.f - fy) * ((1.f - fx) * v00 + fx * v01) + fy * ((1.f - fx) * v10 + fx * v11);
-    out[O_LOC + id] = v;
-}
-
-__global__ __launch_bounds__(256) void kglob2(const float* __restrict__ ws,
-                                              const float* __restrict__ pool_logits,
-                                              const float* __restrict__ mw1,
-                                              const float* __restrict__ mlng,
-                                              const float* __restrict__ mlnb,
-                                              const float* __restrict__ mw2,
-                                              const float* __restrict__ mb2,
-                                              float* __restrict__ out) {
+__global__ __launch_bounds__(256) void ktail(const float* __restrict__ ws,
+                                             const float* __restrict__ pool_logits,
+                                             const float* __restrict__ mw1,
+                                             const float* __restrict__ mlng,
+                                             const float* __restrict__ mlnb,
+                                             const float* __restrict__ mw2,
+                                             const float* __restrict__ mb2,
+                                             float* __restrict__ out) {
     __shared__ float pooled[DD];
     __shared__ float zbuf[HH];
     __shared__ float hbuf[HH];
     __shared__ float sm[4];
-    int lb = blockIdx.x;
-    int l = lb >> 4;
-    int b = lb & 15;
+    int bid = blockIdx.x;
     int t = threadIdx.x;
-    float p0 = pool_logits[l * 2], p1 = pool_logits[l * 2 + 1];
-    float mx = fmaxf(p0, p1);
-    float e0 = expf(p0 - mx), e1 = expf(p1 - mx);
-    float pw0 = e0 / (e0 + e1), pw1 = e1 / (e0 + e1);
-    if (b == 0 && t < 2) out[O_PW + l * 2 + t] = (t == 0) ? pw0 : pw1;
-
-    for (int d = t; d < DD; d += 256) pooled[d] = ws[OFF_PGL + lb * DD + d];
-    __syncthreads();
-    if (t < HH) {
-        const float* wrow = mw1 + (size_t)(l * HH + t) * DD;
-        float a = 0.f;
-        for (int d2 = 0; d2 < DD; d2++) a += pooled[d2] * wrow[d2];
-        zbuf[t] = a;
-    }
-    __syncthreads();
-    float zv = (t < HH) ? zbuf[t] : 0.f;
-    float s1r = blockReduceSum(zv, sm);
-    float s2r = blockReduceSum(zv * zv, sm);
-    float mean = s1r * (1.f / HH);
-    float var = s2r * (1.f / HH) - mean * mean;
-    float rstd = rsqrtf(var + 1e-5f);
-    if (t < HH) {
-        float h = (zbuf[t] - mean) * rstd * mlng[l * HH + t] + mlnb[l * HH + t];
-        hbuf[t] = fmaxf(h, 0.f);
-    }
-    __syncthreads();
-    float hv = (t < HH) ? hbuf[t] : 0.f;
-    float w0v = (t < HH) ? mw2[(size_t)(l * 2 + 0) * HH + t] : 0.f;
-    float w1v = (t < HH) ? mw2[(size_t)(l * 2 + 1) * HH + t] : 0.f;
-    float s0 = blockReduceSum(hv * w0v, sm);
-    float s1 = blockReduceSum(hv * w1v, sm);
-    if (t == 0) out[O_GLG + lb] = (s1 + mb2[l * 2 + 1]) - (s0 + mb2[l * 2]);
+    if (bid < NRESB) {
+        int id = bid * 256 + t;
+        int ox = id % IMGSZ;
+        int tmp = id / IMGSZ;
+        int oy = tmp % IMGSZ;
+        int tmp2 = tmp / IMGSZ;
+        int ch = tmp2 & 1;
+        int lb = tmp2 >> 1;
+        const float S = 64.f / 240.f;
+        float xs = fminf(fmaxf((ox + 0.5f) * S - 0.5f, 0.f), 63.f);
+        float ys = fminf(fmaxf((oy + 0.5f) * S - 0.5f, 0.f), 63.f);
+        int x0 = (int)xs, y0 = (int)ys;
+        float fx = xs - x0, fy = ys - y0;
+        int x1 = min(x0 + 1, 63), y1 = min(y0 + 1, 63);
+        const float* basep = ws + OFF_RAW3 + (size_t)(lb * 2 + ch) * 4096;
+        float v00 = basep[y0 * 64 + x0], v01 = basep[y0 * 64 + x1];
+        float v10 = basep[y1 * 64 + x0], v11 = basep[y1 * 64 + x1];
+        float v = (1.f - fy) * ((1.f - fx) * v00 + fx * v01) + fy * ((1.f - fx) * v10 + fx * v11);
+        out[O_LOC + id] = v;
+        return;
+    }
+    if (bid < NRESB + LBTOT) {
+        int lb = bid - NRESB;
+        int gy = t >> 4, gx = t & 15;
+        const float* r3 = ws + OFF_RAW3 + (size_t)lb * 2 * 4096;
+        float pl[2];
+        #pragma unroll
+        for (int ch = 0; ch < 2; ch++) {
+            const float* basep = r3 + ch * 4096;
+            float s = 0.f;
+            #pragma unroll
+            for (int dy = 0; dy < 4; dy++)
+                #pragma unroll
+                for (int dx = 0; dx < 4; dx++)
+                    s += basep[(gy * 4 + dy) * 64 + gx * 4 + dx];
+            pl[ch] = s * (1.f / 16.f);
+        }
+        out[O_PLG + lb * NNQ + t] = pl[1] - pl[0];
+        out[O_PSC + lb * NNQ + t] = 1.f / (1.f + expf(pl[0] - pl[1]));
+        return;
+    }
+    {
+        int lb = bid - NRESB - LBTOT;
+        int l = lb >> 4;
+        int b = lb & 15;
+        float p0 = pool_logits[l * 2], p1 = pool_logits[l * 2 + 1];
+        float mx = fmaxf(p0, p1);
+        float e0 = expf(p0 - mx), e1 = expf(p1 - mx);
+        float pw0 = e0 / (e0 + e1), pw1 = e1 / (e0 + e1);
+        if (b == 0 && t < 2) out[O_PW + l * 2 + t] = (t == 0) ? pw0 : pw1;
+
+        for (int d = t; d < DD; d += 256) pooled[d] = ws[OFF_PGL + lb * DD + d];
+        __syncthreads();
+        if (t < HH) {
+            const float* wrow = mw1 + (size_t)(l * HH + t) * DD;
+            float a = 0.f;
+            for (int d2 = 0; d2 < DD; d2++) a += pooled[d2] * wrow[d2];
+            zbuf[t] = a;
+        }
+        __syncthreads();
+        float zv = (t < HH) ? zbuf[t] : 0.f;
+        float s1r = blockReduceSum(zv, sm);
+        float s2r = blockReduceSum(zv * zv, sm);
+        float mean = s1r * (1.f / HH);
+        float var = s2r * (1.f / HH) - mean * mean;
+        float rstd = rsqrtf(var + 1e-5f);
+        if (t < HH) {
+            float h = (zbuf[t] - mean) * rstd * mlng[l * HH + t] + mlnb[l * HH + t];
+            hbuf[t] = fmaxf(h, 0.f);
+        }
+        __syncthreads();
+        float hv = (t < HH) ? hbuf[t] : 0.f;
+        float w0v = (t < HH) ? mw2[(size_t)(l * 2 + 0) * HH + t] : 0.f;
+        float w1v = (t < HH) ? mw2[(size_t)(l * 2 + 1) * HH + t] : 0.f;
+        float s0 = blockReduceSum(hv * w0v, sm);
+        float s1 = blockReduceSum(hv * w1v, sm);
+        if (t == 0) out[O_GLG + lb] = (s1 + mb2[l * 2 + 1]) - (s0 + mb2[l * 2]);
+    }
 }
 
 extern "C" void kernel_launch(void* const* d_in, const int* in_sizes, int n_in,
@@ -1008,40 +1017,29 @@
     hipLaunchKernelGGL(knormq, dim3(LLY*BB*NNQ), dim3(192), 0, stream, query, ws);
     hipLaunchKernelGGL(ksimm, dim3(LBTOT*16), dim3(512), 0, stream, prompt, ws);
     hipLaunchKernelGGL(kpost, dim3(LBTOT*16), dim3(256), 0, stream, query, prompt, ws, out);
-    hipLaunchKernelGGL(kbnfin, dim3(LLY*12), dim3(256), 0, stream, sharebn_g, sharebn_b, ws);
-    hipLaunchKernelGGL(kgapf, dim3(LBTOT*12), dim3(64), 0, stream, ws, pool_logits);
+    hipLaunchKernelGGL(kstatsgap, dim3(LBTOT*12), dim3(256), 0, stream,
+                       sharebn_g, sharebn_b, pool_logits, ws);
     hipLaunchKernelGGL(kw1cvt, dim3(LLY*HH), dim3(256), 0, stream, lw1, ws);
     hipLaunchKernelGGL(kbn1cvt, dim3(LBTOT*48), dim3(256), 0, stream, ws);
     hipLaunchKernelGGL(kconv1m, dim3(LBTOT*12), dim3(256), 0, stream, ws);
-    hipLaunchKernelGGL(kc1red, dim3(768), dim3(256), 0, stream, ws);
     hipLaunchKernelGGL(kbnstats, dim3(LLY*HH), dim3(256), 0, stream,
-                       ws + OFF_X1, HH, 256, lbn1g, lbn1b, ws + OFF_BN1);
-    hipLaunchKernelGGL(kxcvt, dim3(LBTOT*8), dim3(256), 0, stream,
-                       ws + OFF_X1, ws + OFF_BN1, (unsigned short*)(ws + OFF_T2) + X1B_SH,
-                       HH, 256, 4, 2);
-    hipLaunchKernelGGL(kwtcvt, dim3(LLY*HH), dim3(128), 0, stream,
-                       lwt1, (unsigned short*)(ws + OFF_T2) + WT1B_SH, HH, HH);
+                       ws + OFF_X1, ws + OFF_C1P, 5, (size_t)LBTOT*HH*256,
+                       HH, 256, lbn1g, lbn1b, ws + OFF_BN1);
+    hipLaunchKernelGGL(kcvtT1, dim3(LBTOT*8 + LLY*HH), dim3(256), 0, stream, lwt1, ws);
     hipLaunchKernelGGL(kconvTm, dim3(LBTOT*4*2), dim3(256), 0, stream,
                        (const unsigned short*)(ws + OFF_T2) + X1B_SH,
                        (const unsigned short*)(ws + OFF_T2) + WT1B_SH,
                        lbt1, ws + OFF_T1, HH, HH, 4, 1, 2);
-    hipLaunchKernelGGL(kt1cvt, dim3(LBTOT*32), dim3(256), 0, stream, ws);
-    hipLaunchKernelGGL(kw2cvt, dim3(LLY*MD), dim3(256), 0, stream, lw2, ws);
+    hipLaunchKernelGGL(kcvtT2mix, dim3(LBTOT*32 + LLY*MD), dim3(256), 0, stream, lw2, ws);
     hipLaunchKernelGGL(kconv2m, dim3(LBTOT*8), dim3(256), 0, stream, ws);
-    hipLaunchKernelGGL(kc2red, dim3(1536), dim3(256), 0, stream, ws);
     hipLaunchKernelGGL(kbnstats, dim3(LLY*MD), dim3(256), 0, stream,
-                       ws + OFF_X2, MD, 1024, lbn2g, lbn2b, ws + OFF_BN2);
-    hipLaunchKernelGGL(kxcvt, dim3(LBTOT*16), dim3(256), 0, stream,
-                       ws + OFF_X2, ws + OFF_BN2, (unsigned short*)(ws + OFF_X1),
-                       MD, 1024, 16, 1);
-    hipLaunchKernelGGL(kwtcvt, dim3(LLY*MD), dim3(128), 0, stream,
-                       lwt2, (unsigned short*)(ws + OFF_X2), MD, MD);
+                       ws + OFF_X2, ws + OFF_C2P, 1, (size_t)0,
+                       MD, 1024, lbn2g, lbn2b, ws + OFF_BN2);
+    hipLaunchKernelGGL(kcvtT2b, dim3(LBTOT*16 + LLY*MD), dim3(256), 0, stream, lwt2, ws);
     hipLaunchKernelGGL(kconvT2f, dim3(LBTOT*4*4), dim3(256), 0, stream,
                        (const unsigned short*)(ws + OFF_X1),
-                       (const unsigned short*)(ws + OFF_X2),
+                       (const unsigned short*)(ws + OFF_WT2B),
                        lbt2, lw3, lb3, ws);
-    hipLaunchKernelGGL(kpool, dim3(LBTOT), dim3(256), 0, stream, ws, out);
-    hipLaunchKernelGGL(kresize, dim3(LLY*BB*2*IMGSZ*IMGSZ/256), dim3(256), 0, stream, ws, out);
-    hipLaunchKernelGGL(kglob2, dim3(LBTOT), dim3(256), 0, stream,
+    hipLaunchKernelGGL(ktail, dim3(NRESB + 2*LBTOT), dim3(256), 0, stream,
                        ws, pool_logits, mw1, mlng, mlnb, mw2, mb2, out);
 }
```

Measured after the change: 493.5 us. About the same (-0.1%).
